# Performance work log

Measured on AMD Instinct MI355X. Metric: run time of the kernel, lower is better.

## Reference

```python
import jax, jax.numpy as jnp
import numpy as np

B, S, H, D = 256, 512, 256, 512  # batch, n_seq, n_hid, n_dim
LN_EPS = 1e-5


def _xavier(key, fan_out, fan_in):
    lim = (6.0 / (fan_in + fan_out)) ** 0.5
    return jax.random.uniform(key, (fan_out, fan_in), jnp.float32, -lim, lim)


def setup_inputs() -> dict:
    key = jax.random.key(0)
    ks = jax.random.split(key, 10)
    x = jax.random.normal(ks[0], (B, S, D), jnp.float32)
    k_w = _xavier(ks[1], H, D)
    q_w = _xavier(ks[2], H, D)
    v_w = _xavier(ks[3], H, D)
    lb = 1.0 / (D ** 0.5)
    k_b = jax.random.uniform(ks[4], (H,), jnp.float32, -lb, lb)
    q_b = jax.random.uniform(ks[5], (H,), jnp.float32, -lb, lb)
    v_b = jax.random.uniform(ks[6], (H,), jnp.float32, -lb, lb)
    attn_bias = jax.random.normal(ks[7], (S, H), jnp.float32)
    ln_g = jnp.ones((H,), jnp.float32)
    ln_b = jnp.zeros((H,), jnp.float32)
    lo = 1.0 / ((S * H) ** 0.5)
    out_w = jax.random.uniform(ks[8], (D, S * H), jnp.float32, -lo, lo)
    out_b = jax.random.uniform(ks[9], (D,), jnp.float32, -lo, lo)
    return {"x": x, "k_w": k_w, "k_b": k_b, "q_w": q_w, "q_b": q_b,
            "v_w": v_w, "v_b": v_b, "attn_bias": attn_bias,
            "ln_g": ln_g, "ln_b": ln_b, "out_w": out_w, "out_b": out_b}


def reference(x, k_w, k_b, q_w, q_b, v_w, v_b, attn_bias, ln_g, ln_b, out_w, out_b):
    # projections: [B,S,D] -> [B,S,H]
    k = jnp.einsum('bsd,hd->bsh', x, k_w) + k_b
    q = jnp.einsum('bsd,hd->bsh', x, q_w) + q_b
    v = jnp.einsum('bsd,hd->bsh', x, v_w) + v_b
    # scores = k^T q, scaled by BATCH size^-0.5 (faithful to v.shape[0]**-0.5)
    scale = x.shape[0] ** (-0.5)
    scores = jnp.einsum('bsh,bsg->bhg', k, q) * scale  # [B,H,H]
    weight = jax.nn.softmax(scores, axis=1)
    out = jnp.einsum('bsh,bhg->bsg', v, weight)  # [B,S,H]
    out = out + attn_bias
    # LayerNorm over last dim
    mu = out.mean(-1, keepdims=True)
    var = out.var(-1, keepdims=True)
    out = (out - mu) * jax.lax.rsqrt(var + LN_EPS) * ln_g + ln_b
    # dropout is identity in eval mode; exact (erf) GELU matches torch default
    out = jax.nn.gelu(out, approximate=False)
    out = out.reshape(out.shape[0], S * H)
    out = out @ out_w.T + out_b  # [B,D]
    return out[:, None, :]  # [B,1,D]
```

## Files before the change

### kernel.cpp

```cpp
#include <hip/hip_runtime.h>
#include <hip/hip_bf16.h>
#include <math.h>

#define B_ 256
#define S_ 512
#define H_ 256
#define D_ 512

typedef __bf16 bf16;
typedef __bf16 bf16x8 __attribute__((ext_vector_type(8)));
typedef float  f32x4  __attribute__((ext_vector_type(4)));
typedef unsigned short u16x8 __attribute__((ext_vector_type(8)));
typedef unsigned short u16x4 __attribute__((ext_vector_type(4)));

#define MFMA(a, b, c) __builtin_amdgcn_mfma_f32_16x16x32_bf16((a), (b), (c), 0, 0, 0)

__device__ __forceinline__ int swz(int row, int kbyte) {
  return (row * 128 + kbyte) ^ ((row & 7) << 4);
}
__device__ __forceinline__ unsigned short bfbits(float f) {
  bf16 h = (bf16)f;
  union { bf16 b; unsigned short u; } c; c.b = h; return c.u;
}
__device__ __forceinline__ bf16x8 cvt8(const float* __restrict__ p) {
  f32x4 a = *(const f32x4*)p;
  f32x4 b = *(const f32x4*)(p + 4);
  bf16x8 r;
  r[0] = (bf16)a[0]; r[1] = (bf16)a[1]; r[2] = (bf16)a[2]; r[3] = (bf16)a[3];
  r[4] = (bf16)b[0]; r[5] = (bf16)b[1]; r[6] = (bf16)b[2]; r[7] = (bf16)b[3];
  return r;
}
__device__ __forceinline__ void gload16(const unsigned short* g, unsigned char* l) {
  __builtin_amdgcn_global_load_lds(
      (const __attribute__((address_space(1))) unsigned int*)g,
      (__attribute__((address_space(3))) unsigned int*)l, 16, 0, 0);
}

__global__ __launch_bounds__(256) void k_convw(
    const float* __restrict__ kw, const float* __restrict__ qw,
    const float* __restrict__ vw, unsigned short* __restrict__ wc)
{
  const int r = blockIdx.x;
  const float* src = (r < 256) ? kw + (size_t)r * 512
                   : (r < 512) ? qw + (size_t)(r - 256) * 512
                               : vw + (size_t)(r - 512) * 512;
  const int c = threadIdx.x * 2;
  wc[(size_t)r * 512 + c]     = bfbits(src[c]);
  wc[(size_t)r * 512 + c + 1] = bfbits(src[c + 1]);
}

__global__ __launch_bounds__(256) void k_convx(
    const float* __restrict__ x, unsigned short* __restrict__ xb, int nchunk)
{
  for (int c = blockIdx.x * 256 + threadIdx.x; c < nchunk; c += gridDim.x * 256) {
    bf16x8 v = cvt8(x + (size_t)c * 8);
    *(bf16x8*)(xb + (size_t)c * 8) = v;
  }
}

__global__ __launch_bounds__(256) void k_proj2(
    const unsigned short* __restrict__ xb,
    const unsigned short* __restrict__ wc,
    const float* __restrict__ kbi, const float* __restrict__ qbi,
    const float* __restrict__ vbi,
    unsigned short* __restrict__ k_t, unsigned short* __restrict__ q_t,
    unsigned short* __restrict__ v_o, int cstart, int nwg)
{
  __shared__ __align__(16) unsigned char sA[16384];
  __shared__ __align__(16) unsigned char sB[16384];

  const int o = blockIdx.x;
  const int cpx = nwg >> 3;
  const int a = (o & 7) * cpx + (o >> 3);
  const int mt = a / 6;
  const int nb = a - mt * 6;
  const int m0 = mt * 128;
  const int n0 = nb * 128;
  const int region = nb >> 1;
  const int h0 = (nb & 1) * 128;
  const float* __restrict__ Bi = (region == 0) ? kbi : (region == 1) ? qbi : vbi;

  const int tid = threadIdx.x;
  const int lane = tid & 63;
  const int wid = tid >> 6;
  const int wm = wid >> 1;
  const int wn = wid & 1;

  f32x4 acc[4][4];
#pragma unroll
  for (int i = 0; i < 4; ++i)
#pragma unroll
    for (int j = 0; j < 4; ++j) acc[i][j] = (f32x4){0.f, 0.f, 0.f, 0.f};

  const int lr = lane >> 3;
  const int lk = (lane & 7) << 3;

  for (int kt = 0; kt < 8; ++kt) {
    if (kt) __syncthreads();
#pragma unroll
    for (int i = 0; i < 4; ++i) {
      const int chunk = wid * 4 + i;
      const int row = chunk * 8 + lr;
      gload16(xb + (size_t)(m0 + row) * 512 + kt * 64 + lk, sA + chunk * 1024);
      gload16(wc + (size_t)(n0 + row) * 512 + kt * 64 + lk, sB + chunk * 1024);
    }
    __syncthreads();
#pragma unroll
    for (int ks = 0; ks < 2; ++ks) {
      const int kb2 = ks * 64 + ((lane >> 4) << 4);
      bf16x8 av[4], bv[4];
#pragma unroll
      for (int f = 0; f < 4; ++f)
        av[f] = *(const bf16x8*)(sA + (wm * 64 + f * 16 + (lane & 15)) * 128 + kb2);
#pragma unroll
      for (int f = 0; f < 4; ++f)
        bv[f] = *(const bf16x8*)(sB + (wn * 64 + f * 16 + (lane & 15)) * 128 + kb2);
#pragma unroll
      for (int fm = 0; fm < 4; ++fm)
#pragma unroll
        for (int fn = 0; fn < 4; ++fn)
          acc[fm][fn] = MFMA(av[fm], bv[fn], acc[fm][fn]);
    }
  }

  const int m0g = cstart * 512 + m0;
  const int b = m0g >> 9;
  const int sbase = m0g & 511;
  const int r4 = (lane >> 4) * 4;
#pragma unroll
  for (int fn = 0; fn < 4; ++fn) {
    const int hcol = h0 + wn * 64 + fn * 16 + (lane & 15);
    const float bias = Bi[hcol];
#pragma unroll
    for (int fm = 0; fm < 4; ++fm) {
      const int s = sbase + wm * 64 + fm * 16 + r4;
      if (region < 2) {
        unsigned short* dst = ((region == 0) ? k_t : q_t) +
                              (size_t)b * (H_ * S_) + (size_t)hcol * S_ + s;
        u16x4 ov;
#pragma unroll
        for (int j = 0; j < 4; ++j) ov[j] = bfbits(acc[fm][fn][j] + bias);
        *(u16x4*)dst = ov;
      } else {
#pragma unroll
        for (int j = 0; j < 4; ++j)
          v_o[(size_t)b * (S_ * H_) + (size_t)(s + j) * H_ + hcol] =
              bfbits(acc[fm][fn][j] + bias);
      }
    }
  }
}

__global__ __launch_bounds__(512) void k_scores(
    const unsigned short* __restrict__ k_t,
    const unsigned short* __restrict__ q_t,
    unsigned short* __restrict__ w_t)
{
  __shared__ __align__(16) unsigned char sA[256 * 128];
  __shared__ __align__(16) unsigned char sB[64 * 128];
  __shared__ float red[4][64];

  const int tid = threadIdx.x;
  const int lane = tid & 63;
  const int wid = tid >> 6;
  const int wm = wid >> 1;
  const int wn = wid & 1;
  const int b = blockIdx.y;
  const int g0 = blockIdx.x * 64;

  const unsigned short* __restrict__ Ab = k_t + (size_t)b * (H_ * S_);
  const unsigned short* __restrict__ Bb = q_t + (size_t)b * (H_ * S_) + (size_t)g0 * S_;

  f32x4 acc[4][2];
#pragma unroll
  for (int i = 0; i < 4; ++i)
#pragma unroll
    for (int j = 0; j < 2; ++j) acc[i][j] = (f32x4){0.f, 0.f, 0.f, 0.f};

  for (int kt = 0; kt < 8; ++kt) {
    __syncthreads();
#pragma unroll
    for (int i = 0; i < 4; ++i) {
      int c = tid + i * 512;
      int row = c >> 3, kc = (c & 7) * 8;
      *(u16x8*)(sA + swz(row, kc * 2)) =
          *(const u16x8*)(Ab + (size_t)row * S_ + kt * 64 + kc);
    }
    {
      int row = tid >> 3, kc = (tid & 7) * 8;
      *(u16x8*)(sB + swz(row, kc * 2)) =
          *(const u16x8*)(Bb + (size_t)row * S_ + kt * 64 + kc);
    }
    __syncthreads();
#pragma unroll
    for (int ks = 0; ks < 2; ++ks) {
      const int kbyte = ks * 64 + (lane >> 4) * 16;
      bf16x8 av[4], bv[2];
#pragma unroll
      for (int f = 0; f < 4; ++f)
        av[f] = *(const bf16x8*)(sA + swz(wm * 64 + f * 16 + (lane & 15), kbyte));
#pragma unroll
      for (int f = 0; f < 2; ++f)
        bv[f] = *(const bf16x8*)(sB + swz(wn * 32 + f * 16 + (lane & 15), kbyte));
#pragma unroll
      for (int fm = 0; fm < 4; ++fm)
#pragma unroll
        for (int fn = 0; fn < 2; ++fn)
          acc[fm][fn] = MFMA(av[fm], bv[fn], acc[fm][fn]);
    }
  }

#pragma unroll
  for (int fm = 0; fm < 4; ++fm)
#pragma unroll
    for (int fn = 0; fn < 2; ++fn)
#pragma unroll
      for (int j = 0; j < 4; ++j) acc[fm][fn][j] *= 0.0625f;

  float cmax[2] = {-3.0e38f, -3.0e38f};
#pragma unroll
  for (int fm = 0; fm < 4; ++fm)
#pragma unroll
    for (int fn = 0; fn < 2; ++fn)
#pragma unroll
      for (int j = 0; j < 4; ++j) cmax[fn] = fmaxf(cmax[fn], acc[fm][fn][j]);
  cmax[0] = fmaxf(cmax[0], __shfl_xor(cmax[0], 16));
  cmax[1] = fmaxf(cmax[1], __shfl_xor(cmax[1], 16));
  cmax[0] = fmaxf(cmax[0], __shfl_xor(cmax[0], 32));
  cmax[1] = fmaxf(cmax[1], __shfl_xor(cmax[1], 32));
  if (lane < 16) {
    red[wm][wn * 32 + lane] = cmax[0];
    red[wm][wn * 32 + 16 + lane] = cmax[1];
  }
  __syncthreads();
  float gmax[2];
#pragma unroll
  for (int fn = 0; fn < 2; ++fn) {
    int c = wn * 32 + fn * 16 + (lane & 15);
    gmax[fn] = fmaxf(fmaxf(red[0][c], red[1][c]), fmaxf(red[2][c], red[3][c]));
  }
  __syncthreads();
  float csum[2] = {0.f, 0.f};
#pragma unroll
  for (int fm = 0; fm < 4; ++fm)
#pragma unroll
    for (int fn = 0; fn < 2; ++fn)
#pragma unroll
      for (int j = 0; j < 4; ++j) {
        float p = __expf(acc[fm][fn][j] - gmax[fn]);
        acc[fm][fn][j] = p;
        csum[fn] += p;
      }
  csum[0] += __shfl_xor(csum[0], 16);
  csum[1] += __shfl_xor(csum[1], 16);
  csum[0] += __shfl_xor(csum[0], 32);
  csum[1] += __shfl_xor(csum[1], 32);
  if (lane < 16) {
    red[wm][wn * 32 + lane] = csum[0];
    red[wm][wn * 32 + 16 + lane] = csum[1];
  }
  __syncthreads();
  const int r4 = (lane >> 4) * 4;
#pragma unroll
  for (int fn = 0; fn < 2; ++fn) {
    int c = wn * 32 + fn * 16 + (lane & 15);
    float ginv = 1.0f / (red[0][c] + red[1][c] + red[2][c] + red[3][c]);
    int g = g0 + c;
#pragma unroll
    for (int fm = 0; fm < 4; ++fm) {
      int h = wm * 64 + fm * 16 + r4;
      u16x4 ov;
#pragma unroll
      for (int j = 0; j < 4; ++j) ov[j] = bfbits(acc[fm][fn][j] * ginv);
      *(u16x4*)(w_t + (size_t)b * (H_ * H_) + (size_t)g * H_ + h) = ov;
    }
  }
}

__global__ __launch_bounds__(512) void k_pv(
    const unsigned short* __restrict__ v_o,
    const unsigned short* __restrict__ w_t,
    const float* __restrict__ attn_bias,
    const float* __restrict__ lng,
    const float* __restrict__ lnb,
    unsigned short* __restrict__ act)
{
  __shared__ __align__(16) unsigned char sA[128 * 128];
  __shared__ __align__(16) unsigned char sB[256 * 128];
  __shared__ float lbuf[2][4][128];

  const int tid = threadIdx.x;
  const int lane = tid & 63;
  const int wid = tid >> 6;
  const int wm = wid >> 2;
  const int wn = wid & 3;
  const int b = blockIdx.y;
  const int s0 = blockIdx.x * 128;

  const unsigned short* __restrict__ Ab = v_o + (size_t)b * (S_ * H_) + (size_t)s0 * H_;
  const unsigned short* __restrict__ Bb = w_t + (size_t)b * (H_ * H_);

  f32x4 acc[4][4];
#pragma unroll
  for (int i = 0; i < 4; ++i)
#pragma unroll
    for (int j = 0; j < 4; ++j) acc[i][j] = (f32x4){0.f, 0.f, 0.f, 0.f};

  for (int kt = 0; kt < 4; ++kt) {
    __syncthreads();
#pragma unroll
    for (int i = 0; i < 2; ++i) {
      int c = tid + i * 512;
      int row = c >> 3, kc = (c & 7) * 8;
      *(u16x8*)(sA + swz(row, kc * 2)) =
          *(const u16x8*)(Ab + (size_t)row * H_ + kt * 64 + kc);
    }
#pragma unroll
    for (int i = 0; i < 4; ++i) {
      int c = tid + i * 512;
      int row = c >> 3, kc = (c & 7) * 8;
      *(u16x8*)(sB + swz(row, kc * 2)) =
          *(const u16x8*)(Bb + (size_t)row * H_ + kt * 64 + kc);
    }
    __syncthreads();
#pragma unroll
    for (int ks = 0; ks < 2; ++ks) {
      const int kbyte = ks * 64 + (lane >> 4) * 16;
      bf16x8 av[4], bv[4];
#pragma unroll
      for (int f = 0; f < 4; ++f)
        av[f] = *(const bf16x8*)(sA + swz(wm * 64 + f * 16 + (lane & 15), kbyte));
#pragma unroll
      for (int f = 0; f < 4; ++f)
        bv[f] = *(const bf16x8*)(sB + swz(wn * 64 + f * 16 + (lane & 15), kbyte));
#pragma unroll
      for (int fm = 0; fm < 4; ++fm)
#pragma unroll
        for (int fn = 0; fn < 4; ++fn)
          acc[fm][fn] = MFMA(av[fm], bv[fn], acc[fm][fn]);
    }
  }

  const int r4 = (lane >> 4) * 4;
  float lg[4], lb[4];
#pragma unroll
  for (int fn = 0; fn < 4; ++fn) {
    int g = wn * 64 + fn * 16 + (lane & 15);
    lg[fn] = lng[g];
    lb[fn] = lnb[g];
  }
#pragma unroll
  for (int fm = 0; fm < 4; ++fm) {
#pragma unroll
    for (int j = 0; j < 4; ++j) {
      const int rloc = wm * 64 + fm * 16 + r4 + j;
      const int sl = s0 + rloc;
      float ps = 0.f, psq = 0.f;
#pragma unroll
      for (int fn = 0; fn < 4; ++fn) {
        int g = wn * 64 + fn * 16 + (lane & 15);
        float vv = acc[fm][fn][j] + attn_bias[(size_t)sl * H_ + g];
        acc[fm][fn][j] = vv;
        ps += vv;
        psq += vv * vv;
      }
      ps += __shfl_xor(ps, 1);  psq += __shfl_xor(psq, 1);
      ps += __shfl_xor(ps, 2);  psq += __shfl_xor(psq, 2);
      ps += __shfl_xor(ps, 4);  psq += __shfl_xor(psq, 4);
      ps += __shfl_xor(ps, 8);  psq += __shfl_xor(psq, 8);
      if ((lane & 15) == 0) { lbuf[0][wn][rloc] = ps; lbuf[1][wn][rloc] = psq; }
    }
  }
  __syncthreads();
#pragma unroll
  for (int fm = 0; fm < 4; ++fm) {
#pragma unroll
    for (int j = 0; j < 4; ++j) {
      const int rloc = wm * 64 + fm * 16 + r4 + j;
      float sum = lbuf[0][0][rloc] + lbuf[0][1][rloc] + lbuf[0][2][rloc] + lbuf[0][3][rloc];
      float sq  = lbuf[1][0][rloc] + lbuf[1][1][rloc] + lbuf[1][2][rloc] + lbuf[1][3][rloc];
      float mu = sum * (1.f / H_);
      float var = sq * (1.f / H_) - mu * mu;
      float rstd = rsqrtf(var + 1e-5f);
      const int sl = s0 + rloc;
#pragma unroll
      for (int fn = 0; fn < 4; ++fn) {
        int g = wn * 64 + fn * 16 + (lane & 15);
        float xv = (acc[fm][fn][j] - mu) * rstd * lg[fn] + lb[fn];
        float y = 0.5f * xv * (1.f + erff(xv * 0.70710678118654752f));
        act[(size_t)b * (S_ * H_) + (size_t)sl * H_ + g] = bfbits(y);
      }
    }
  }
}

__global__ __launch_bounds__(512) void k_final(
    const unsigned short* __restrict__ act,
    const float* __restrict__ ow,
    float* __restrict__ partial)
{
  __shared__ __align__(16) unsigned char sA[256 * 128];
  __shared__ __align__(16) unsigned char sB[64 * 128];

  const int tid = threadIdx.x;
  const int lane = tid & 63;
  const int wid = tid >> 6;
  const int wm = wid >> 1;
  const int wn = wid & 1;
  const int n0 = blockIdx.x * 64;
  const size_t k0 = (size_t)blockIdx.y * 4096;

  f32x4 acc[4][2];
#pragma unroll
  for (int i = 0; i < 4; ++i)
#pragma unroll
    for (int j = 0; j < 2; ++j) acc[i][j] = (f32x4){0.f, 0.f, 0.f, 0.f};

  for (int kt = 0; kt < 64; ++kt) {
    const size_t kb = k0 + kt * 64;
    __syncthreads();
#pragma unroll
    for (int i = 0; i < 4; ++i) {
      int c = tid + i * 512;
      int row = c >> 3, kc = (c & 7) * 8;
      *(u16x8*)(sA + swz(row, kc * 2)) =
          *(const u16x8*)(act + (size_t)row * 131072 + kb + kc);
    }
    {
      int row = tid >> 3, kc = (tid & 7) * 8;
      *(bf16x8*)(sB + swz(row, kc * 2)) =
          cvt8(ow + (size_t)(n0 + row) * 131072 + kb + kc);
    }
    __syncthreads();
#pragma unroll
    for (int ks = 0; ks < 2; ++ks) {
      const int kbyte = ks * 64 + (lane >> 4) * 16;
      bf16x8 av[4], bv[2];
#pragma unroll
      for (int f = 0; f < 4; ++f)
        av[f] = *(const bf16x8*)(sA + swz(wm * 64 + f * 16 + (lane & 15), kbyte));
#pragma unroll
      for (int f = 0; f < 2; ++f)
        bv[f] = *(const bf16x8*)(sB + swz(wn * 32 + f * 16 + (lane & 15), kbyte));
#pragma unroll
      for (int fm = 0; fm < 4; ++fm)
#pragma unroll
        for (int fn = 0; fn < 2; ++fn)
          acc[fm][fn] = MFMA(av[fm], bv[fn], acc[fm][fn]);
    }
  }

  float* __restrict__ P = partial + (size_t)blockIdx.y * (256 * 512);
  const int r4 = (lane >> 4) * 4;
#pragma unroll
  for (int fn = 0; fn < 2; ++fn) {
    int col = n0 + wn * 32 + fn * 16 + (lane & 15);
#pragma unroll
    for (int fm = 0; fm < 4; ++fm) {
      int mb = wm * 64 + fm * 16 + r4;
#pragma unroll
      for (int j = 0; j < 4; ++j)
        P[(size_t)(mb + j) * 512 + col] = acc[fm][fn][j];
    }
  }
}

__global__ __launch_bounds__(256) void k_reduce(
    const float* __restrict__ partial,
    const float* __restrict__ ob,
    float* __restrict__ out)
{
  const int i4 = blockIdx.x * 256 + threadIdx.x;
  f32x4 s = *(const f32x4*)(ob + ((i4 & 127) << 2));
#pragma unroll
  for (int ks = 0; ks < 32; ++ks)
    s += *(const f32x4*)(partial + (size_t)ks * 131072 + (size_t)i4 * 4);
  *(f32x4*)(out + (size_t)i4 * 4) = s;
}

extern "C" void kernel_launch(void* const* d_in, const int* in_sizes, int n_in,
                              void* d_out, int out_size, void* d_ws, size_t ws_size,
                              hipStream_t stream) {
  const float* x         = (const float*)d_in[0];
  const float* k_w       = (const float*)d_in[1];
  const float* k_b       = (const float*)d_in[2];
  const float* q_w       = (const float*)d_in[3];
  const float* q_b       = (const float*)d_in[4];
  const float* v_w       = (const float*)d_in[5];
  const float* v_b       = (const float*)d_in[6];
  const float* attn_bias = (const float*)d_in[7];
  const float* ln_g      = (const float*)d_in[8];
  const float* ln_b      = (const float*)d_in[9];
  const float* out_w     = (const float*)d_in[10];
  const float* out_b     = (const float*)d_in[11];
  float* out = (float*)d_out;

  char* ws = (char*)d_ws;
  unsigned short* k_t = (unsigned short*)(ws);
  unsigned short* q_t = (unsigned short*)(ws + 67108864);
  unsigned short* v_o = (unsigned short*)(ws + 134217728);
  unsigned short* wc  = (unsigned short*)(ws + 201326592);
  unsigned short* xb  = (unsigned short*)(ws + 201326592 + 786432);
  unsigned short* w_t = (unsigned short*)(ws + 201326592);
  unsigned short* act = k_t;
  float* partial      = (float*)(ws + 67108864);

  k_convw<<<dim3(768), dim3(256), 0, stream>>>(k_w, q_w, v_w, wc);

  const int starts[5] = {0, 56, 112, 168, 224};
  const int nbats[5]  = {56, 56, 56, 56, 32};
  for (int r = 0; r < 5; ++r) {
    const int nbat = nbats[r];
    k_convx<<<dim3(1024), dim3(256), 0, stream>>>(
        x + (size_t)starts[r] * 262144, xb, nbat * 32768);
    const int nwg = nbat * 24;
    k_proj2<<<dim3(nwg), dim3(256), 0, stream>>>(
        xb, wc, k_b, q_b, v_b, k_t, q_t, v_o, starts[r], nwg);
  }

  k_scores<<<dim3(4, 256), dim3(512), 0, stream>>>(k_t, q_t, w_t);
  k_pv<<<dim3(4, 256), dim3(512), 0, stream>>>(
      v_o, w_t, attn_bias, ln_g, ln_b, act);
  k_final<<<dim3(8, 32), dim3(512), 0, stream>>>(act, out_w, partial);
  k_reduce<<<dim3(128), dim3(256), 0, stream>>>(partial, out_b, out);
}
```

Baseline: 551.6 us.

## Fuse scores, softmax, PV, LayerNorm and GELU into one per-batch kernel

Merges the score/softmax kernel and the PV/LayerNorm/GELU kernel into a single kernel with one workgroup per batch. The normalized softmax matrix is kept in a 128KB swizzled LDS buffer instead of being written to and read back from global memory. V fragments are read straight from global memory rather than staged through LDS. This removes the global round trip for the weight matrix and one kernel launch, but drops the grid to 256 large workgroups and raises register and LDS pressure, which can limit latency hiding.

```diff
diff --git a/kernel.cpp b/kernel.cpp
--- a/kernel.cpp
+++ b/kernel.cpp
@@ -17,6 +17,9 @@
 
 __device__ __forceinline__ int swz(int row, int kbyte) {
   return (row * 128 + kbyte) ^ ((row & 7) << 4);
+}
+__device__ __forceinline__ int pswz(int row, int kbyte) {
+  return (row * 512 + kbyte) ^ ((row & 7) << 4);
 }
 __device__ __forceinline__ unsigned short bfbits(float f) {
   bf16 h = (bf16)f;
@@ -151,31 +154,42 @@
   }
 }
 
-__global__ __launch_bounds__(512) void k_scores(
+__global__ __launch_bounds__(512, 2) void k_attn(
     const unsigned short* __restrict__ k_t,
     const unsigned short* __restrict__ q_t,
-    unsigned short* __restrict__ w_t)
+    const unsigned short* __restrict__ v_o,
+    const float* __restrict__ attn_bias,
+    const float* __restrict__ lng, const float* __restrict__ lnb,
+    unsigned short* __restrict__ act)
 {
-  __shared__ __align__(16) unsigned char sA[256 * 128];
-  __shared__ __align__(16) unsigned char sB[64 * 128];
-  __shared__ float red[4][64];
+  __shared__ __align__(16) unsigned char sP[131072];
+  __shared__ float lbuf[2][4][128];
 
   const int tid = threadIdx.x;
   const int lane = tid & 63;
   const int wid = tid >> 6;
-  const int wm = wid >> 1;
-  const int wn = wid & 1;
-  const int b = blockIdx.y;
-  const int g0 = blockIdx.x * 64;
-
-  const unsigned short* __restrict__ Ab = k_t + (size_t)b * (H_ * S_);
-  const unsigned short* __restrict__ Bb = q_t + (size_t)b * (H_ * S_) + (size_t)g0 * S_;
-
-  f32x4 acc[4][2];
-#pragma unroll
-  for (int i = 0; i < 4; ++i)
-#pragma unroll
-    for (int j = 0; j < 2; ++j) acc[i][j] = (f32x4){0.f, 0.f, 0.f, 0.f};
+  const int b = blockIdx.x;
+  const int l15 = lane & 15;
+  const int l16 = lane >> 4;
+  const int r4 = l16 * 4;
+
+  const unsigned short* __restrict__ Kb = k_t + (size_t)b * (H_ * S_);
+  const unsigned short* __restrict__ Qb = q_t + (size_t)b * (H_ * S_);
+  const unsigned short* __restrict__ Vb = v_o + (size_t)b * (S_ * H_);
+
+  unsigned char* sK = sP;
+  unsigned char* sQ = sP + 32768;
+  float* redm = (float*)(sP + 65536);
+  float* reds = (float*)(sP + 67584);
+
+  const int wh = wid >> 2;
+  const int wg = wid & 3;
+
+  f32x4 acc1[8][4];
+#pragma unroll
+  for (int i = 0; i < 8; ++i)
+#pragma unroll
+    for (int j = 0; j < 4; ++j) acc1[i][j] = (f32x4){0.f, 0.f, 0.f, 0.f};
 
   for (int kt = 0; kt < 8; ++kt) {
     __syncthreads();
@@ -183,212 +197,179 @@
     for (int i = 0; i < 4; ++i) {
       int c = tid + i * 512;
       int row = c >> 3, kc = (c & 7) * 8;
-      *(u16x8*)(sA + swz(row, kc * 2)) =
-          *(const u16x8*)(Ab + (size_t)row * S_ + kt * 64 + kc);
-    }
-    {
-      int row = tid >> 3, kc = (tid & 7) * 8;
-      *(u16x8*)(sB + swz(row, kc * 2)) =
-          *(const u16x8*)(Bb + (size_t)row * S_ + kt * 64 + kc);
+      *(u16x8*)(sK + swz(row, kc * 2)) =
+          *(const u16x8*)(Kb + (size_t)row * S_ + kt * 64 + kc);
+      *(u16x8*)(sQ + swz(row, kc * 2)) =
+          *(const u16x8*)(Qb + (size_t)row * S_ + kt * 64 + kc);
     }
     __syncthreads();
 #pragma unroll
     for (int ks = 0; ks < 2; ++ks) {
-      const int kbyte = ks * 64 + (lane >> 4) * 16;
-      bf16x8 av[4], bv[2];
+      const int kbyte = ks * 64 + l16 * 16;
+      bf16x8 av[8], bv[4];
+#pragma unroll
+      for (int f = 0; f < 8; ++f)
+        av[f] = *(const bf16x8*)(sK + swz(wh * 128 + f * 16 + l15, kbyte));
 #pragma unroll
       for (int f = 0; f < 4; ++f)
-        av[f] = *(const bf16x8*)(sA + swz(wm * 64 + f * 16 + (lane & 15), kbyte));
-#pragma unroll
-      for (int f = 0; f < 2; ++f)
-        bv[f] = *(const bf16x8*)(sB + swz(wn * 32 + f * 16 + (lane & 15), kbyte));
-#pragma unroll
-      for (int fm = 0; fm < 4; ++fm)
-#pragma unroll
-        for (int fn = 0; fn < 2; ++fn)
-          acc[fm][fn] = MFMA(av[fm], bv[fn], acc[fm][fn]);
-    }
-  }
-
-#pragma unroll
-  for (int fm = 0; fm < 4; ++fm)
-#pragma unroll
-    for (int fn = 0; fn < 2; ++fn)
-#pragma unroll
-      for (int j = 0; j < 4; ++j) acc[fm][fn][j] *= 0.0625f;
-
-  float cmax[2] = {-3.0e38f, -3.0e38f};
-#pragma unroll
-  for (int fm = 0; fm < 4; ++fm)
-#pragma unroll
-    for (int fn = 0; fn < 2; ++fn)
-#pragma unroll
-      for (int j = 0; j < 4; ++j) cmax[fn] = fmaxf(cmax[fn], acc[fm][fn][j]);
-  cmax[0] = fmaxf(cmax[0], __shfl_xor(cmax[0], 16));
-  cmax[1] = fmaxf(cmax[1], __shfl_xor(cmax[1], 16));
-  cmax[0] = fmaxf(cmax[0], __shfl_xor(cmax[0], 32));
-  cmax[1] = fmaxf(cmax[1], __shfl_xor(cmax[1], 32));
+        bv[f] = *(const bf16x8*)(sQ + swz(wg * 64 + f * 16 + l15, kbyte));
+#pragma unroll
+      for (int fm = 0; fm < 8; ++fm)
+#pragma unroll
+        for (int fn = 0; fn < 4; ++fn)
+          acc1[fm][fn] = MFMA(av[fm], bv[fn], acc1[fm][fn]);
+    }
+  }
+
+#pragma unroll
+  for (int fm = 0; fm < 8; ++fm)
+#pragma unroll
+    for (int fn = 0; fn < 4; ++fn)
+#pragma unroll
+      for (int j = 0; j < 4; ++j) acc1[fm][fn][j] *= 0.0625f;
+
+  float cmax[4] = {-3.0e38f, -3.0e38f, -3.0e38f, -3.0e38f};
+#pragma unroll
+  for (int fm = 0; fm < 8; ++fm)
+#pragma unroll
+    for (int fn = 0; fn < 4; ++fn)
+#pragma unroll
+      for (int j = 0; j < 4; ++j) cmax[fn] = fmaxf(cmax[fn], acc1[fm][fn][j]);
+#pragma unroll
+  for (int fn = 0; fn < 4; ++fn) {
+    cmax[fn] = fmaxf(cmax[fn], __shfl_xor(cmax[fn], 16));
+    cmax[fn] = fmaxf(cmax[fn], __shfl_xor(cmax[fn], 32));
+  }
   if (lane < 16) {
-    red[wm][wn * 32 + lane] = cmax[0];
-    red[wm][wn * 32 + 16 + lane] = cmax[1];
+#pragma unroll
+    for (int fn = 0; fn < 4; ++fn)
+      redm[wh * 256 + wg * 64 + fn * 16 + lane] = cmax[fn];
   }
   __syncthreads();
-  float gmax[2];
-#pragma unroll
-  for (int fn = 0; fn < 2; ++fn) {
-    int c = wn * 32 + fn * 16 + (lane & 15);
-    gmax[fn] = fmaxf(fmaxf(red[0][c], red[1][c]), fmaxf(red[2][c], red[3][c]));
-  }
-  __syncthreads();
-  float csum[2] = {0.f, 0.f};
-#pragma unroll
-  for (int fm = 0; fm < 4; ++fm)
-#pragma unroll
-    for (int fn = 0; fn < 2; ++fn)
+  float gmax[4];
+#pragma unroll
+  for (int fn = 0; fn < 4; ++fn) {
+    int c = wg * 64 + fn * 16 + l15;
+    gmax[fn] = fmaxf(redm[c], redm[256 + c]);
+  }
+  float csum[4] = {0.f, 0.f, 0.f, 0.f};
+#pragma unroll
+  for (int fm = 0; fm < 8; ++fm)
+#pragma unroll
+    for (int fn = 0; fn < 4; ++fn)
 #pragma unroll
       for (int j = 0; j < 4; ++j) {
-        float p = __expf(acc[fm][fn][j] - gmax[fn]);
-        acc[fm][fn][j] = p;
+        float p = __expf(acc1[fm][fn][j] - gmax[fn]);
+        acc1[fm][fn][j] = p;
         csum[fn] += p;
       }
-  csum[0] += __shfl_xor(csum[0], 16);
-  csum[1] += __shfl_xor(csum[1], 16);
-  csum[0] += __shfl_xor(csum[0], 32);
-  csum[1] += __shfl_xor(csum[1], 32);
+#pragma unroll
+  for (int fn = 0; fn < 4; ++fn) {
+    csum[fn] += __shfl_xor(csum[fn], 16);
+    csum[fn] += __shfl_xor(csum[fn], 32);
+  }
   if (lane < 16) {
-    red[wm][wn * 32 + lane] = csum[0];
-    red[wm][wn * 32 + 16 + lane] = csum[1];
+#pragma unroll
+    for (int fn = 0; fn < 4; ++fn)
+      reds[wh * 256 + wg * 64 + fn * 16 + lane] = csum[fn];
   }
   __syncthreads();
-  const int r4 = (lane >> 4) * 4;
-#pragma unroll
-  for (int fn = 0; fn < 2; ++fn) {
-    int c = wn * 32 + fn * 16 + (lane & 15);
-    float ginv = 1.0f / (red[0][c] + red[1][c] + red[2][c] + red[3][c]);
-    int g = g0 + c;
+  float ginv[4];
+#pragma unroll
+  for (int fn = 0; fn < 4; ++fn) {
+    int c = wg * 64 + fn * 16 + l15;
+    ginv[fn] = 1.0f / (reds[c] + reds[256 + c]);
+  }
+  __syncthreads();
+
+#pragma unroll
+  for (int fn = 0; fn < 4; ++fn) {
+    const int g = wg * 64 + fn * 16 + l15;
+#pragma unroll
+    for (int fm = 0; fm < 8; ++fm) {
+      const int h = wh * 128 + fm * 16 + r4;
+      u16x4 pv;
+#pragma unroll
+      for (int j = 0; j < 4; ++j) pv[j] = bfbits(acc1[fm][fn][j] * ginv[fn]);
+      *(u16x4*)(sP + pswz(g, h * 2)) = pv;
+    }
+  }
+  __syncthreads();
+
+  const float* __restrict__ bias = attn_bias;
+  for (int ms = 0; ms < 4; ++ms) {
+    const int s0 = ms * 128 + wh * 64;
+    f32x4 acc2[4][4];
+#pragma unroll
+    for (int i = 0; i < 4; ++i)
+#pragma unroll
+      for (int j = 0; j < 4; ++j) acc2[i][j] = (f32x4){0.f, 0.f, 0.f, 0.f};
+
+#pragma unroll
+    for (int kt = 0; kt < 4; ++kt) {
+      bf16x8 av[4][2];
+#pragma unroll
+      for (int fm = 0; fm < 4; ++fm)
+#pragma unroll
+        for (int ks = 0; ks < 2; ++ks)
+          av[fm][ks] = *(const bf16x8*)(
+              Vb + (size_t)(s0 + fm * 16 + l15) * H_ + kt * 64 + ks * 32 + l16 * 8);
+#pragma unroll
+      for (int ks = 0; ks < 2; ++ks) {
+        bf16x8 bv[4];
+#pragma unroll
+        for (int fn = 0; fn < 4; ++fn)
+          bv[fn] = *(const bf16x8*)(
+              sP + pswz(wg * 64 + fn * 16 + l15, kt * 128 + ks * 64 + l16 * 16));
+#pragma unroll
+        for (int fm = 0; fm < 4; ++fm)
+#pragma unroll
+          for (int fn = 0; fn < 4; ++fn)
+            acc2[fm][fn] = MFMA(av[fm][ks], bv[fn], acc2[fm][fn]);
+      }
+    }
+
+    __syncthreads();
 #pragma unroll
     for (int fm = 0; fm < 4; ++fm) {
-      int h = wm * 64 + fm * 16 + r4;
-      u16x4 ov;
-#pragma unroll
-      for (int j = 0; j < 4; ++j) ov[j] = bfbits(acc[fm][fn][j] * ginv);
-      *(u16x4*)(w_t + (size_t)b * (H_ * H_) + (size_t)g * H_ + h) = ov;
-    }
-  }
-}
-
-__global__ __launch_bounds__(512) void k_pv(
-    const unsigned short* __restrict__ v_o,
-    const unsigned short* __restrict__ w_t,
-    const float* __restrict__ attn_bias,
-    const float* __restrict__ lng,
-    const float* __restrict__ lnb,
-    unsigned short* __restrict__ act)
-{
-  __shared__ __align__(16) unsigned char sA[128 * 128];
-  __shared__ __align__(16) unsigned char sB[256 * 128];
-  __shared__ float lbuf[2][4][128];
-
-  const int tid = threadIdx.x;
-  const int lane = tid & 63;
-  const int wid = tid >> 6;
-  const int wm = wid >> 2;
-  const int wn = wid & 3;
-  const int b = blockIdx.y;
-  const int s0 = blockIdx.x * 128;
-
-  const unsigned short* __restrict__ Ab = v_o + (size_t)b * (S_ * H_) + (size_t)s0 * H_;
-  const unsigned short* __restrict__ Bb = w_t + (size_t)b * (H_ * H_);
-
-  f32x4 acc[4][4];
-#pragma unroll
-  for (int i = 0; i < 4; ++i)
-#pragma unroll
-    for (int j = 0; j < 4; ++j) acc[i][j] = (f32x4){0.f, 0.f, 0.f, 0.f};
-
-  for (int kt = 0; kt < 4; ++kt) {
-    __syncthreads();
-#pragma unroll
-    for (int i = 0; i < 2; ++i) {
-      int c = tid + i * 512;
-      int row = c >> 3, kc = (c & 7) * 8;
-      *(u16x8*)(sA + swz(row, kc * 2)) =
-          *(const u16x8*)(Ab + (size_t)row * H_ + kt * 64 + kc);
-    }
-#pragma unroll
-    for (int i = 0; i < 4; ++i) {
-      int c = tid + i * 512;
-      int row = c >> 3, kc = (c & 7) * 8;
-      *(u16x8*)(sB + swz(row, kc * 2)) =
-          *(const u16x8*)(Bb + (size_t)row * H_ + kt * 64 + kc);
-    }
-    __syncthreads();
-#pragma unroll
-    for (int ks = 0; ks < 2; ++ks) {
-      const int kbyte = ks * 64 + (lane >> 4) * 16;
-      bf16x8 av[4], bv[4];
-#pragma unroll
-      for (int f = 0; f < 4; ++f)
-        av[f] = *(const bf16x8*)(sA + swz(wm * 64 + f * 16 + (lane & 15), kbyte));
-#pragma unroll
-      for (int f = 0; f < 4; ++f)
-        bv[f] = *(const bf16x8*)(sB + swz(wn * 64 + f * 16 + (lane & 15), kbyte));
-#pragma unroll
-      for (int fm = 0; fm < 4; ++fm)
-#pragma unroll
-        for (int fn = 0; fn < 4; ++fn)
-          acc[fm][fn] = MFMA(av[fm], bv[fn], acc[fm][fn]);
-    }
-  }
-
-  const int r4 = (lane >> 4) * 4;
-  float lg[4], lb[4];
-#pragma unroll
-  for (int fn = 0; fn < 4; ++fn) {
-    int g = wn * 64 + fn * 16 + (lane & 15);
-    lg[fn] = lng[g];
-    lb[fn] = lnb[g];
-  }
-#pragma unroll
-  for (int fm = 0; fm < 4; ++fm) {
-#pragma unroll
-    for (int j = 0; j < 4; ++j) {
-      const int rloc = wm * 64 + fm * 16 + r4 + j;
-      const int sl = s0 + rloc;
-      float ps = 0.f, psq = 0.f;
-#pragma unroll
-      for (int fn = 0; fn < 4; ++fn) {
-        int g = wn * 64 + fn * 16 + (lane & 15);
-        float vv = acc[fm][fn][j] + attn_bias[(size_t)sl * H_ + g];
-        acc[fm][fn][j] = vv;
-        ps += vv;
-        psq += vv * vv;
+#pragma unroll
+      for (int j = 0; j < 4; ++j) {
+        const int rloc = wh * 64 + fm * 16 + r4 + j;
+        const int s = ms * 128 + rloc;
+        float ps = 0.f, psq = 0.f;
+#pragma unroll
+        for (int fn = 0; fn < 4; ++fn) {
+          int g = wg * 64 + fn * 16 + l15;
+          float vv = acc2[fm][fn][j] + bias[(size_t)s * H_ + g];
+          acc2[fm][fn][j] = vv;
+          ps += vv; psq += vv * vv;
+        }
+        ps += __shfl_xor(ps, 1);  psq += __shfl_xor(psq, 1);
+        ps += __shfl_xor(ps, 2);  psq += __shfl_xor(psq, 2);
+        ps += __shfl_xor(ps, 4);  psq += __shfl_xor(psq, 4);
+        ps += __shfl_xor(ps, 8);  psq += __shfl_xor(psq, 8);
+        if (l15 == 0) { lbuf[0][wg][rloc] = ps; lbuf[1][wg][rloc] = psq; }
       }
-      ps += __shfl_xor(ps, 1);  psq += __shfl_xor(psq, 1);
-      ps += __shfl_xor(ps, 2);  psq += __shfl_xor(psq, 2);
-      ps += __shfl_xor(ps, 4);  psq += __shfl_xor(psq, 4);
-      ps += __shfl_xor(ps, 8);  psq += __shfl_xor(psq, 8);
-      if ((lane & 15) == 0) { lbuf[0][wn][rloc] = ps; lbuf[1][wn][rloc] = psq; }
-    }
-  }
-  __syncthreads();
-#pragma unroll
-  for (int fm = 0; fm < 4; ++fm) {
-#pragma unroll
-    for (int j = 0; j < 4; ++j) {
-      const int rloc = wm * 64 + fm * 16 + r4 + j;
-      float sum = lbuf[0][0][rloc] + lbuf[0][1][rloc] + lbuf[0][2][rloc] + lbuf[0][3][rloc];
-      float sq  = lbuf[1][0][rloc] + lbuf[1][1][rloc] + lbuf[1][2][rloc] + lbuf[1][3][rloc];
-      float mu = sum * (1.f / H_);
-      float var = sq * (1.f / H_) - mu * mu;
-      float rstd = rsqrtf(var + 1e-5f);
-      const int sl = s0 + rloc;
-#pragma unroll
-      for (int fn = 0; fn < 4; ++fn) {
-        int g = wn * 64 + fn * 16 + (lane & 15);
-        float xv = (acc[fm][fn][j] - mu) * rstd * lg[fn] + lb[fn];
-        float y = 0.5f * xv * (1.f + erff(xv * 0.70710678118654752f));
-        act[(size_t)b * (S_ * H_) + (size_t)sl * H_ + g] = bfbits(y);
+    }
+    __syncthreads();
+#pragma unroll
+    for (int fm = 0; fm < 4; ++fm) {
+#pragma unroll
+      for (int j = 0; j < 4; ++j) {
+        const int rloc = wh * 64 + fm * 16 + r4 + j;
+        const int s = ms * 128 + rloc;
+        float sum = lbuf[0][0][rloc] + lbuf[0][1][rloc] + lbuf[0][2][rloc] + lbuf[0][3][rloc];
+        float sq  = lbuf[1][0][rloc] + lbuf[1][1][rloc] + lbuf[1][2][rloc] + lbuf[1][3][rloc];
+        float mu = sum * (1.f / H_);
+        float var = sq * (1.f / H_) - mu * mu;
+        float rstd = rsqrtf(var + 1e-5f);
+#pragma unroll
+        for (int fn = 0; fn < 4; ++fn) {
+          int g = wg * 64 + fn * 16 + l15;
+          float xv = (acc2[fm][fn][j] - mu) * rstd * lng[g] + lnb[g];
+          float y = 0.5f * xv * (1.f + erff(xv * 0.70710678118654752f));
+          act[(size_t)b * (S_ * H_) + (size_t)s * H_ + g] = bfbits(y);
+        }
       }
     }
   }
@@ -501,7 +482,6 @@
   unsigned short* v_o = (unsigned short*)(ws + 134217728);
   unsigned short* wc  = (unsigned short*)(ws + 201326592);
   unsigned short* xb  = (unsigned short*)(ws + 201326592 + 786432);
-  unsigned short* w_t = (unsigned short*)(ws + 201326592);
   unsigned short* act = k_t;
   float* partial      = (float*)(ws + 67108864);
 
@@ -518,9 +498,9 @@
         xb, wc, k_b, q_b, v_b, k_t, q_t, v_o, starts[r], nwg);
   }
 
-  k_scores<<<dim3(4, 256), dim3(512), 0, stream>>>(k_t, q_t, w_t);
-  k_pv<<<dim3(4, 256), dim3(512), 0, stream>>>(
-      v_o, w_t, attn_bias, ln_g, ln_b, act);
+  k_attn<<<dim3(256), dim3(512), 0, stream>>>(
+      k_t, q_t, v_o, attn_bias, ln_g, ln_b, act);
+
   k_final<<<dim3(8, 32), dim3(512), 0, stream>>>(act, out_w, partial);
   k_reduce<<<dim3(128), dim3(256), 0, stream>>>(partial, out_b, out);
 }
```

After: 517.8 us. 1.07x faster.
